# Optimization experiments

Hardware: AMD Instinct MI355X
Metric: run time of the kernel (lower is better)

Reference implementation:

```python
import jax, jax.numpy as jnp
import numpy as np

V, D, H, L, DF = 32000, 768, 12, 12, 3072
B, S, BS = 2, 1024, 16
MASK_ID = V - 1
HD = D // H
STD = 0.02


def setup_inputs() -> dict:
    key = jax.random.key(0)
    ks = jax.random.split(key, 12)
    ids = jax.random.randint(ks[0], (B, S), 0, V)
    m = jax.random.uniform(ks[1], (B, S)) < 0.15
    input_ids = jnp.where(m, MASK_ID, ids)
    target_ids = jax.random.randint(ks[2], (B, S), 0, V)
    noise_level = jax.random.uniform(ks[3], (B,), minval=0.1, maxval=1.0)
    emb = jax.random.normal(ks[4], (V, D)) * STD
    in_w = jax.random.normal(ks[5], (L, 3 * D, D)) * STD
    in_b = jnp.zeros((L, 3 * D))
    attn_out_w = jax.random.normal(ks[6], (L, D, D)) * STD
    attn_out_b = jnp.zeros((L, D))
    ln1_w = jnp.ones((L, D)); ln1_b = jnp.zeros((L, D))
    ln2_w = jnp.ones((L, D)); ln2_b = jnp.zeros((L, D))
    w1 = jax.random.normal(ks[7], (L, DF, D)) * STD; b1 = jnp.zeros((L, DF))
    w2 = jax.random.normal(ks[8], (L, D, DF)) * STD; b2 = jnp.zeros((L, D))
    proj_w = jax.random.normal(ks[9], (V, D)) * STD; proj_b = jnp.zeros((V,))
    return dict(input_ids=input_ids, target_ids=target_ids, noise_level=noise_level,
                emb=emb, in_w=in_w, in_b=in_b, attn_out_w=attn_out_w, attn_out_b=attn_out_b,
                ln1_w=ln1_w, ln1_b=ln1_b, ln2_w=ln2_w, ln2_b=ln2_b,
                w1=w1, b1=b1, w2=w2, b2=b2, proj_w=proj_w, proj_b=proj_b)


def _ln(x, w, b):
    m = x.mean(-1, keepdims=True)
    v = ((x - m) ** 2).mean(-1, keepdims=True)
    return (x - m) / jnp.sqrt(v + 1e-5) * w + b


def _rotary(x):
    # Vectorized equivalent of the per-scalar torch loop: rotates pairs
    # (0,1),(2,3),... within the first rotary_dim = D//2 channels only.
    rd = D // 2
    freqs = 1.0 / (10000.0 ** (jnp.arange(0, rd, 2, dtype=jnp.float32) / rd))  # [rd//2]
    ang = jnp.arange(S, dtype=jnp.float32)[:, None] * freqs[None, :]           # [S, rd//2]
    cos, sin = jnp.cos(ang), jnp.sin(ang)
    xr = x[..., :rd].reshape(B, S, rd // 2, 2)
    x0, x1 = xr[..., 0], xr[..., 1]
    r0 = x0 * cos - x1 * sin
    r1 = x0 * sin + x1 * cos
    rot = jnp.stack([r0, r1], axis=-1).reshape(B, S, rd)
    return jnp.concatenate([rot, x[..., rd:]], axis=-1)


def _block_causal_mask():
    nb = S // BS
    bm = jnp.tril(jnp.ones((nb, nb), dtype=jnp.float32))
    em = jnp.repeat(jnp.repeat(bm, BS, axis=0), BS, axis=1)  # [S, S]
    return (1.0 - em) * -1e9


def _model(input_ids, target_ids, noise_level, emb, in_w, in_b, attn_out_w, attn_out_b,
           ln1_w, ln1_b, ln2_w, ln2_b, w1, b1, w2, b2, proj_w, proj_b):
    x = emb[input_ids]                 # [B, S, D]
    x = _rotary(x)
    mask = _block_causal_mask()        # [S, S] additive
    scale = 1.0 / jnp.sqrt(jnp.float32(HD))
    for l in range(L):
        h = _ln(x, ln1_w[l], ln1_b[l])
        qkv = h @ in_w[l].T + in_b[l]
        q, k, v = jnp.split(qkv, 3, axis=-1)
        q = q.reshape(B, S, H, HD).transpose(0, 2, 1, 3)
        k = k.reshape(B, S, H, HD).transpose(0, 2, 1, 3)
        v = v.reshape(B, S, H, HD).transpose(0, 2, 1, 3)
        scores = jnp.einsum('bhqd,bhkd->bhqk', q, k) * scale + mask
        a = jax.nn.softmax(scores, axis=-1)
        o = jnp.einsum('bhqk,bhkd->bhqd', a, v).transpose(0, 2, 1, 3).reshape(B, S, D)
        x = x + (o @ attn_out_w[l].T + attn_out_b[l])
        h = _ln(x, ln2_w[l], ln2_b[l])
        x = x + (jax.nn.gelu(h @ w1[l].T + b1[l], approximate=False) @ w2[l].T + b2[l])
    logits = x @ proj_w.T + proj_b     # [B, S, V]
    logp = jax.nn.log_softmax(logits, axis=-1)
    ce = -jnp.take_along_axis(logp, target_ids[..., None], axis=-1)[..., 0]  # [B, S]
    is_masked = (input_ids == MASK_ID).astype(logits.dtype)
    weighted = ce * is_masked / noise_level[:, None]
    loss = weighted.sum() / (is_masked.sum() + 1e-8)
    return loss, logits


def reference(input_ids, target_ids, noise_level, emb, in_w, in_b, attn_out_w, attn_out_b,
              ln1_w, ln1_b, ln2_w, ln2_b, w1, b1, w2, b2, proj_w, proj_b):
    return _model(input_ids, target_ids, noise_level, emb, in_w, in_b, attn_out_w, attn_out_b,
                  ln1_w, ln1_b, ln2_w, ln2_b, w1, b1, w2, b2, proj_w, proj_b)
```

## Files before the change

### kernel.cpp

```cpp
#include <hip/hip_runtime.h>
#include <hip/hip_bf16.h>
#include <math.h>

#define V_SZ 32000
#define D_SZ 768
#define H_SZ 12
#define L_SZ 12
#define DF_SZ 3072
#define B_SZ 2
#define S_SZ 1024
#define BS_SZ 16
#define HD_SZ 64
#define MASK_ID 31999
#define NTOK (B_SZ * S_SZ)

typedef __attribute__((ext_vector_type(8))) short bf16x8;
typedef __attribute__((ext_vector_type(4))) short bf16x4;
typedef __attribute__((ext_vector_type(4))) float f32x4;

union B8 { bf16x8 v; __hip_bfloat162 h[4]; };
union B4 { bf16x4 v; __hip_bfloat162 h[2]; };
union U4 { ushort4 u; __hip_bfloat162 h[2]; };
union U4E { ushort4 u; unsigned short e[4]; };

__device__ inline unsigned short f2bf(float x) {
    __hip_bfloat16 b = __float2bfloat16(x);
    union { __hip_bfloat16 b; unsigned short u; } c; c.b = b;
    return c.u;
}

__global__ __launch_bounds__(256) void conv_fold_kernel(
    const float* __restrict__ Wsrc, const float* __restrict__ lnw,
    const float* __restrict__ lnb, const float* __restrict__ bsrc,
    unsigned short* __restrict__ Wdst, float* __restrict__ bdst,
    int rows_per_layer)
{
    const int gw = (blockIdx.x * 256 + threadIdx.x) >> 6;
    const int lane = threadIdx.x & 63;
    const int l = gw / rows_per_layer;
    const float* src = Wsrc + (size_t)gw * D_SZ;
    const float* wv = lnw + l * D_SZ;
    const float* bv = lnb + l * D_SZ;
    unsigned short* dst = Wdst + (size_t)gw * D_SZ;
    float acc = 0.f;
#pragma unroll
    for (int j = 0; j < 3; ++j) {
        int k = lane * 4 + j * 256;
        float4 s = *(const float4*)(src + k);
        float4 w = *(const float4*)(wv + k);
        float4 bb = *(const float4*)(bv + k);
        acc += bb.x * s.x + bb.y * s.y + bb.z * s.z + bb.w * s.w;
        U4 o;
        o.h[0] = __float22bfloat162_rn(float2{s.x * w.x, s.y * w.y});
        o.h[1] = __float22bfloat162_rn(float2{s.z * w.z, s.w * w.w});
        *(ushort4*)(dst + k) = o.u;
    }
#pragma unroll
    for (int off = 32; off; off >>= 1) acc += __shfl_xor(acc, off);
    if (lane == 0) bdst[gw] = bsrc[gw] + acc;
}

__global__ __launch_bounds__(256) void conv_cast_kernel(
    const float* __restrict__ src, unsigned short* __restrict__ dst, int n8)
{
    int i = blockIdx.x * 256 + threadIdx.x;
    if (i >= n8) return;
    const float* p = src + (size_t)i * 8;
    float4 v0 = *(const float4*)p;
    float4 v1 = *(const float4*)(p + 4);
    B8 r;
    r.h[0] = __float22bfloat162_rn(float2{v0.x, v0.y});
    r.h[1] = __float22bfloat162_rn(float2{v0.z, v0.w});
    r.h[2] = __float22bfloat162_rn(float2{v1.x, v1.y});
    r.h[3] = __float22bfloat162_rn(float2{v1.z, v1.w});
    *(bf16x8*)(dst + (size_t)i * 8) = r.v;
}

__global__ __launch_bounds__(256) void embed_rot_kernel(
    const int* __restrict__ ids, const float* __restrict__ emb,
    float* __restrict__ x)
{
    const int tok = blockIdx.x;
    const int s = tok & (S_SZ - 1);
    const int id = ids[tok];
    const float* e = emb + (size_t)id * D_SZ;
    float* xo = x + (size_t)tok * D_SZ;
    const int t = threadIdx.x;

    if (t < 192) {
        float x0 = e[2 * t], x1 = e[2 * t + 1];
        float freq = powf(10000.f, -((float)(2 * t)) / 384.f);
        float ang = (float)s * freq;
        float sn, cs;
        sincosf(ang, &sn, &cs);
        xo[2 * t]     = x0 * cs - x1 * sn;
        xo[2 * t + 1] = x0 * sn + x1 * cs;
    }
    for (int ch = 384 + t; ch < D_SZ; ch += 256) xo[ch] = e[ch];
}

template<int BM, int BN, int AM, int CM, bool WB16, bool XSWZ, bool CEP, int SPLITK>
__global__ __launch_bounds__(256) void mfma_gemm(
    const void* __restrict__ Av, const void* __restrict__ Wv,
    const float* __restrict__ bias, const float* __restrict__ Res,
    float* __restrict__ C,
    unsigned short* __restrict__ qp, unsigned short* __restrict__ kp,
    unsigned short* __restrict__ vp, float2* __restrict__ pm,
    int M, int N, int K)
{
    constexpr int MR = BM / 32;
    constexpr int NR = BN / 32;
    constexpr int ACH = BM * 4 / 256;
    constexpr int BCH = BN * 4 / 256;

    __shared__ __align__(16) unsigned short As[2][BM * 32];
    __shared__ __align__(16) unsigned short Bs[2][BN * 32];
    __shared__ float smean[AM == 1 ? BM : 1];
    __shared__ float srstd[AM == 1 ? BM : 1];

    const int tid = threadIdx.x;
    const int lane = tid & 63;
    const int wave = tid >> 6;
    const int wrow0 = (wave >> 1) * (BM / 2);
    const int wcol0 = (wave & 1) * (BN / 2);
    const int kgrp = lane >> 4;
    const int rc = lane & 15;
    const int dsw = ((kgrp - (rc >> 1)) & 3) * 8;

    int m0, n0;
    if constexpr (XSWZ) {
        int id = blockIdx.y * gridDim.x + blockIdx.x;
        int cpx = (gridDim.x * gridDim.y) >> 3;
        int swz = (id & 7) * cpx + (id >> 3);
        m0 = (swz % gridDim.x) * BM;
        n0 = (swz / gridDim.x) * BN;
    } else {
        m0 = blockIdx.x * BM;
        n0 = blockIdx.y * BN;
    }
    const int kdiv = K / SPLITK;
    const int kbase = (SPLITK > 1) ? blockIdx.z * kdiv : 0;

    if constexpr (AM == 1) {
        const float* A = (const float*)Av;
        const int row = tid >> 2, q = tid & 3;
        const float* xr = A + (size_t)(m0 + row) * K + q * (K >> 2);
        float sum = 0.f, ss = 0.f;
        for (int j = 0; j < (K >> 4); ++j) {
            float4 v = *(const float4*)(xr + j * 4);
            sum += v.x + v.y + v.z + v.w;
            ss += v.x * v.x + v.y * v.y + v.z * v.z + v.w * v.w;
        }
        sum += __shfl_xor(sum, 1); sum += __shfl_xor(sum, 2);
        ss  += __shfl_xor(ss, 1);  ss  += __shfl_xor(ss, 2);
        float mean = sum * (1.f / (float)K);
        float var = ss * (1.f / (float)K) - mean * mean;
        if (q == 0) { smean[row] = mean; srstd[row] = rsqrtf(var + 1e-5f); }
        __syncthreads();
    }

    f32x4 acc[MR][NR];
#pragma unroll
    for (int i = 0; i < MR; ++i)
#pragma unroll
        for (int j = 0; j < NR; ++j) acc[i][j] = (f32x4){0.f, 0.f, 0.f, 0.f};

    float areg[(AM != 2) ? ACH : 1][8];
    bf16x8 areg16[(AM == 2) ? ACH : 1];
    float bregf[WB16 ? 1 : BCH][8];
    bf16x8 breg16[WB16 ? BCH : 1];

    auto load_a = [&](int k0) {
#pragma unroll
        for (int i = 0; i < ACH; ++i) {
            int c = tid + i * 256;
            int row = c >> 2, ksg = ((c & 3) + (c >> 3)) & 3;
            if constexpr (AM == 2) {
                const unsigned short* A16 = (const unsigned short*)Av;
                areg16[i] = *(const bf16x8*)(A16 + (size_t)(m0 + row) * K + k0 + ksg * 8);
            } else {
                const float* p = (const float*)Av + (size_t)(m0 + row) * K + k0 + ksg * 8;
                float4 v0 = *(const float4*)p;
                float4 v1 = *(const float4*)(p + 4);
                areg[i][0] = v0.x; areg[i][1] = v0.y; areg[i][2] = v0.z; areg[i][3] = v0.w;
                areg[i][4] = v1.x; areg[i][5] = v1.y; areg[i][6] = v1.z; areg[i][7] = v1.w;
            }
        }
    };
    auto write_a = [&](int buf) {
#pragma unroll
        for (int i = 0; i < ACH; ++i) {
            int c = tid + i * 256;
            if constexpr (AM == 2) {
                *(bf16x8*)&As[buf][c * 8] = areg16[i];
            } else {
                int row = c >> 2;
                float sc = 1.f, sh = 0.f;
                if constexpr (AM == 1) { sc = srstd[row]; sh = -smean[row] * sc; }
                B8 r;
                r.h[0] = __float22bfloat162_rn(float2{fmaf(areg[i][0], sc, sh), fmaf(areg[i][1], sc, sh)});
                r.h[1] = __float22bfloat162_rn(float2{fmaf(areg[i][2], sc, sh), fmaf(areg[i][3], sc, sh)});
                r.h[2] = __float22bfloat162_rn(float2{fmaf(areg[i][4], sc, sh), fmaf(areg[i][5], sc, sh)});
                r.h[3] = __float22bfloat162_rn(float2{fmaf(areg[i][6], sc, sh), fmaf(areg[i][7], sc, sh)});
                *(bf16x8*)&As[buf][c * 8] = r.v;
            }
        }
    };

    auto load_b = [&](int k0) {
#pragma unroll
        for (int i = 0; i < BCH; ++i) {
            int c = tid + i * 256;
            int row = c >> 2, ksg = ((c & 3) + (c >> 3)) & 3;
            if constexpr (WB16) {
                const unsigned short* W16 = (const unsigned short*)Wv;
                breg16[i] = *(const bf16x8*)(W16 + (size_t)(n0 + row) * K + k0 + ksg * 8);
            } else {
                const float* p = (const float*)Wv + (size_t)(n0 + row) * K + k0 + ksg * 8;
                float4 v0 = *(const float4*)p;
                float4 v1 = *(const float4*)(p + 4);
                bregf[i][0] = v0.x; bregf[i][1] = v0.y; bregf[i][2] = v0.z; bregf[i][3] = v0.w;
                bregf[i][4] = v1.x; bregf[i][5] = v1.y; bregf[i][6] = v1.z; bregf[i][7] = v1.w;
            }
        }
    };
    auto write_b = [&](int buf) {
#pragma unroll
        for (int i = 0; i < BCH; ++i) {
            int c = tid + i * 256;
            if constexpr (WB16) {
                *(bf16x8*)&Bs[buf][c * 8] = breg16[i];
            } else {
                B8 r;
                r.h[0] = __float22bfloat162_rn(float2{bregf[i][0], bregf[i][1]});
                r.h[1] = __float22bfloat162_rn(float2{bregf[i][2], bregf[i][3]});
                r.h[2] = __float22bfloat162_rn(float2{bregf[i][4], bregf[i][5]});
                r.h[3] = __float22bfloat162_rn(float2{bregf[i][6], bregf[i][7]});
                *(bf16x8*)&Bs[buf][c * 8] = r.v;
            }
        }
    };

    auto compute = [&](int buf) {
        bf16x8 af[MR], bf[NR];
#pragma unroll
        for (int mi = 0; mi < MR; ++mi)
            af[mi] = *(const bf16x8*)&As[buf][(wrow0 + mi * 16 + rc) * 32 + dsw];
#pragma unroll
        for (int ni = 0; ni < NR; ++ni)
            bf[ni] = *(const bf16x8*)&Bs[buf][(wcol0 + ni * 16 + rc) * 32 + dsw];
#pragma unroll
        for (int mi = 0; mi < MR; ++mi)
#pragma unroll
            for (int ni = 0; ni < NR; ++ni)
                acc[mi][ni] = __builtin_amdgcn_mfma_f32_16x16x32_bf16(
                    af[mi], bf[ni], acc[mi][ni], 0, 0, 0);
    };

    load_a(kbase);
    load_b(kbase);
    write_a(0);
    write_b(0);
    __syncthreads();

    const int nk = kdiv >> 5;
    int cur = 0;
    for (int s = 0; s < nk; ++s) {
        const bool more = (s + 1 < nk);
        const int k1 = kbase + ((s + 1) << 5);
        if (more) { load_a(k1); load_b(k1); }
        compute(cur);
        if (more) { write_a(cur ^ 1); write_b(cur ^ 1); }
        __syncthreads();
        cur ^= 1;
    }

#pragma unroll
    for (int mi = 0; mi < MR; ++mi) {
#pragma unroll
        for (int ni = 0; ni < NR; ++ni) {
            const int col = n0 + wcol0 + ni * 16 + rc;
            const int rbase = m0 + wrow0 + mi * 16 + kgrp * 4;
            if constexpr (CM == 1) {
                float bv = bias[col];
                const int region = col / 768;
                const int c768 = col - region * 768;
                const int hh = c768 >> 6, d = c768 & 63;
                const int bb = rbase >> 10, s0 = rbase & 1023;
                const int bh = bb * H_SZ + hh;
                if (region == 0) {
#pragma unroll
                    for (int i = 0; i < 4; ++i)
                        qp[((size_t)(bh << 10) + s0 + i) * 64 + d]
                            = f2bf((acc[mi][ni][i] + bv) * 0.125f);
                } else if (region == 1) {
#pragma unroll
                    for (int i = 0; i < 4; ++i)
                        kp[((size_t)(bh << 10) + s0 + i) * 64 + d]
                            = f2bf(acc[mi][ni][i] + bv);
                } else {
                    U4E t4;
#pragma unroll
                    for (int i = 0; i < 4; ++i) t4.e[i] = f2bf(acc[mi][ni][i] + bv);
                    *(ushort4*)&vp[(((size_t)bh * 64 + d) << 10) + s0] = t4.u;
                }
            } else if constexpr (CM == 2) {
                float bv = bias[col];
                unsigned short* C16 = (unsigned short*)C;
#pragma unroll
                for (int i = 0; i < 4; ++i) {
                    float v = acc[mi][ni][i] + bv;
                    v = 0.5f * v * (1.f + erff(v * 0.70710678118654752f));
                    C16[(size_t)(rbase + i) * N + col] = f2bf(v);
                }
            } else if constexpr (CM == 3) {
                float* P = C + (size_t)blockIdx.z * ((size_t)M * N);
                size_t basei = (size_t)rbase * N + col;
#pragma unroll
                for (int i = 0; i < 4; ++i)
                    P[basei + (size_t)i * N] = acc[mi][ni][i];
            } else {
                float bv = bias ? bias[col] : 0.f;
                size_t basei = (size_t)rbase * N + col;
#pragma unroll
                for (int i = 0; i < 4; ++i) {
                    float v = acc[mi][ni][i] + bv;
                    size_t idx = basei + (size_t)i * N;
                    if (Res) v += Res[idx];
                    C[idx] = v;
                }
            }
        }
    }

    if constexpr (CEP) {
        float2 (*sce)[2] = (float2 (*)[2])As;
        float bvv[NR];
#pragma unroll
        for (int ni = 0; ni < NR; ++ni) bvv[ni] = bias[n0 + wcol0 + ni * 16 + rc];
#pragma unroll
        for (int mi = 0; mi < MR; ++mi) {
#pragma unroll
            for (int i = 0; i < 4; ++i) {
                float vmax = -1e30f;
#pragma unroll
                for (int ni = 0; ni < NR; ++ni)
                    vmax = fmaxf(vmax, acc[mi][ni][i] + bvv[ni]);
                vmax = fmaxf(vmax, __shfl_xor(vmax, 1));
                vmax = fmaxf(vmax, __shfl_xor(vmax, 2));
                vmax = fmaxf(vmax, __shfl_xor(vmax, 4));
                vmax = fmaxf(vmax, __shfl_xor(vmax, 8));
                float ssum = 0.f;
#pragma unroll
                for (int ni = 0; ni < NR; ++ni)
                    ssum += __expf(acc[mi][ni][i] + bvv[ni] - vmax);
                ssum += __shfl_xor(ssum, 1);
                ssum += __shfl_xor(ssum, 2);
                ssum += __shfl_xor(ssum, 4);
                ssum += __shfl_xor(ssum, 8);
                if (rc == 0)
                    sce[wrow0 + mi * 16 + kgrp * 4 + i][wave & 1] = float2{vmax, ssum};
            }
        }
        __syncthreads();
        if (tid < BM) {
            float2 a = sce[tid][0], b2 = sce[tid][1];
            float Mv = fmaxf(a.x, b2.x);
            float Sv = a.y * __expf(a.x - Mv) + b2.y * __expf(b2.x - Mv);
            pm[(size_t)(n0 >> 7) * NTOK + m0 + tid] = float2{Mv, Sv};
        }
    }
}

__global__ __launch_bounds__(256) void ffn2_reduce_kernel(
    const float* __restrict__ pp, const float* __restrict__ bias,
    float* __restrict__ x)
{
    const size_t i = (size_t)(blockIdx.x * 256 + threadIdx.x) * 8;
    const int col = (int)(i % 768);
    const size_t E = (size_t)NTOK * D_SZ;
    float4 s0 = *(const float4*)(x + i);
    float4 s1 = *(const float4*)(x + i + 4);
    float4 b0 = *(const float4*)(bias + col);
    float4 b1 = *(const float4*)(bias + col + 4);
    s0.x += b0.x; s0.y += b0.y; s0.z += b0.z; s0.w += b0.w;
    s1.x += b1.x; s1.y += b1.y; s1.z += b1.z; s1.w += b1.w;
#pragma unroll
    for (int z = 0; z < 2; ++z) {
        float4 p0 = *(const float4*)(pp + z * E + i);
        float4 p1 = *(const float4*)(pp + z * E + i + 4);
        s0.x += p0.x; s0.y += p0.y; s0.z += p0.z; s0.w += p0.w;
        s1.x += p1.x; s1.y += p1.y; s1.z += p1.z; s1.w += p1.w;
    }
    *(float4*)(x + i) = s0;
    *(float4*)(x + i + 4) = s1;
}

__global__ __launch_bounds__(256) void attn3_kernel(
    const unsigned short* __restrict__ Q16, const unsigned short* __restrict__ K16,
    const unsigned short* __restrict__ VT16, unsigned short* __restrict__ ao16)
{
    const int bid = blockIdx.x;
    const int qb = 63 - bid / 24;
    const int bh = bid % 24;
    const int b = bh / H_SZ, h = bh % H_SZ;
    const int tid = threadIdx.x;
    const int w = tid >> 6, lane = tid & 63;
    const int g = lane >> 4, r = lane & 15;

    constexpr int KS = 72;
    __shared__ __align__(16) unsigned short Pl[4][16 * KS];
    __shared__ float so[4][16][66];
    __shared__ float2 sml[4][16];

    const unsigned short* Qb = Q16 + ((size_t)bh << 10) * 64;
    const unsigned short* Kb = K16 + ((size_t)bh << 10) * 64;
    const unsigned short* Vb = VT16 + ((size_t)bh << 6) * 1024;

    bf16x8 qf[2];
    qf[0] = *(const bf16x8*)&Qb[(qb * 16 + r) * 64 + 8 * g];
    qf[1] = *(const bf16x8*)&Qb[(qb * 16 + r) * 64 + 32 + 8 * g];

    float m_r = -1e30f, l_r = 0.f;
    f32x4 o[4];
#pragma unroll
    for (int ni = 0; ni < 4; ++ni) o[ni] = (f32x4){0.f, 0.f, 0.f, 0.f};

    const int nch = (qb >> 2) + 1;
    const int qbm = qb & 3;

    for (int c = w; c < nch; c += 4) {
        const bool lastc = (c == nch - 1);
        const int mi_hi = lastc ? qbm : 3;

        f32x4 s[4];
#pragma unroll
        for (int mi = 0; mi < 4; ++mi) s[mi] = (f32x4){0.f, 0.f, 0.f, 0.f};
#pragma unroll
        for (int mi = 0; mi < 4; ++mi) {
            if (mi <= mi_hi) {
#pragma unroll
                for (int ks = 0; ks < 2; ++ks) {
                    bf16x8 af = *(const bf16x8*)&Kb[(c * 64 + 16 * mi + r) * 64 + 32 * ks + 8 * g];
                    s[mi] = __builtin_amdgcn_mfma_f32_16x16x32_bf16(af, qf[ks], s[mi], 0, 0, 0);
                }
            }
        }

        float mx = -1e30f;
#pragma unroll
        for (int mi = 0; mi < 4; ++mi) {
            if (mi <= mi_hi) {
#pragma unroll
                for (int i = 0; i < 4; ++i) mx = fmaxf(mx, s[mi][i]);
            }
        }
        mx = fmaxf(mx, __shfl_xor(mx, 16));
        mx = fmaxf(mx, __shfl_xor(mx, 32));
        float m_new = fmaxf(m_r, mx);
        float corr = __expf(m_r - m_new);

        float p[4][4];
        float psum = 0.f;
#pragma unroll
        for (int mi = 0; mi < 4; ++mi) {
#pragma unroll
            for (int i = 0; i < 4; ++i) {
                float pv = (mi <= mi_hi) ? __expf(s[mi][i] - m_new) : 0.f;
                p[mi][i] = pv;
                psum += pv;
            }
        }
        psum += __shfl_xor(psum, 16);
        psum += __shfl_xor(psum, 32);
        l_r = l_r * corr + psum;
        m_r = m_new;

#pragma unroll
        for (int mi = 0; mi < 4; ++mi) {
            B4 t;
            t.h[0] = __float22bfloat162_rn(float2{p[mi][0], p[mi][1]});
            t.h[1] = __float22bfloat162_rn(float2{p[mi][2], p[mi][3]});
            *(bf16x4*)&Pl[w][r * KS + 16 * mi + 4 * g] = t.v;
        }

        float co[4];
#pragma unroll
        for (int i = 0; i < 4; ++i) co[i] = __shfl(corr, 4 * g + i);
#pragma unroll
        for (int ni = 0; ni < 4; ++ni)
#pragma unroll
            for (int i = 0; i < 4; ++i) o[ni][i] *= co[i];

#pragma unroll
        for (int ks = 0; ks < 2; ++ks) {
            if (!lastc || 2 * ks <= qbm) {
                bf16x8 pf = *(const bf16x8*)&Pl[w][r * KS + 32 * ks + 8 * g];
#pragma unroll
                for (int ni = 0; ni < 4; ++ni) {
                    bf16x8 vf = *(const bf16x8*)&Vb[(size_t)(r + 16 * ni) * 1024 + c * 64 + 32 * ks + 8 * g];
                    o[ni] = __builtin_amdgcn_mfma_f32_16x16x32_bf16(pf, vf, o[ni], 0, 0, 0);
                }
            }
        }
    }

    if (g == 0) sml[w][r] = float2{m_r, l_r};
#pragma unroll
    for (int ni = 0; ni < 4; ++ni)
#pragma unroll
        for (int i = 0; i < 4; ++i)
            so[w][4 * g + i][r + 16 * ni] = o[ni][i];
    __syncthreads();

#pragma unroll
    for (int j = 0; j < 4; ++j) {
        int e = tid + j * 256;
        int row = e >> 6, col = e & 63;
        float2 p0 = sml[0][row], p1 = sml[1][row], p2 = sml[2][row], p3 = sml[3][row];
        float M = fmaxf(fmaxf(p0.x, p1.x), fmaxf(p2.x, p3.x));
        float w0 = __expf(p0.x - M), w1 = __expf(p1.x - M);
        float w2 = __expf(p2.x - M), w3 = __expf(p3.x - M);
        float L = p0.y * w0 + p1.y * w1 + p2.y * w2 + p3.y * w3;
        float ov = so[0][row][col] * w0 + so[1][row][col] * w1
                 + so[2][row][col] * w2 + so[3][row][col] * w3;
        ao16[(size_t)(b * S_SZ + qb * 16 + row) * D_SZ + h * HD_SZ + col]
            = f2bf(ov / L);
    }
}

__global__ __launch_bounds__(256) void ce2_kernel(
    const float* __restrict__ logits, const int* __restrict__ tgt,
    const int* __restrict__ inp, const float* __restrict__ noise,
    float* __restrict__ ce_row, float* __restrict__ msk_row)
{
    const int row = blockIdx.x;
    const int t = threadIdx.x;
    const float* lr = logits + (size_t)row * V_SZ;
    const float4* lr4 = (const float4*)lr;

    float m = -1e30f, s = 0.f;
    for (int i = t; i < V_SZ / 4; i += 256) {
        float4 v = lr4[i];
        float mx4 = fmaxf(fmaxf(v.x, v.y), fmaxf(v.z, v.w));
        if (mx4 > m) { s *= __expf(m - mx4); m = mx4; }
        s += __expf(v.x - m) + __expf(v.y - m) + __expf(v.z - m) + __expf(v.w - m);
    }

    __shared__ float sm[256], ss[256];
    sm[t] = m; ss[t] = s;
    __syncthreads();
    for (int off = 128; off; off >>= 1) {
        if (t < off) {
            float m2 = fmaxf(sm[t], sm[t + off]);
            ss[t] = ss[t] * __expf(sm[t] - m2) + ss[t + off] * __expf(sm[t + off] - m2);
            sm[t] = m2;
        }
        __syncthreads();
    }
    if (t == 0) {
        float M = sm[0], S = ss[0];
        int tg = tgt[row];
        float ce = -(lr[tg] - M - logf(S));
        int ism = (inp[row] == MASK_ID) ? 1 : 0;
        int b = row / S_SZ;
        ce_row[row] = ism ? (ce / noise[b]) : 0.f;
        msk_row[row] = ism ? 1.f : 0.f;
    }
}

__global__ __launch_bounds__(64) void ce3_kernel(
    const float2* __restrict__ pm, const float* __restrict__ logits,
    const int* __restrict__ tgt, const int* __restrict__ inp,
    const float* __restrict__ noise, float* __restrict__ ce_row,
    float* __restrict__ msk_row)
{
    const int row = blockIdx.x * 64 + threadIdx.x;
    float m = -1e30f, s = 0.f;
    for (int bb = 0; bb < V_SZ / 128; ++bb) {
        float2 p = pm[(size_t)bb * NTOK + row];
        float M2 = fmaxf(m, p.x);
        s = s * __expf(m - M2) + p.y * __expf(p.x - M2);
        m = M2;
    }
    int tg = tgt[row];
    float lv = logits[(size_t)row * V_SZ + tg];
    float ce = -(lv - m - logf(s));
    int ism = (inp[row] == MASK_ID) ? 1 : 0;
    int b = row / S_SZ;
    ce_row[row] = ism ? (ce / noise[b]) : 0.f;
    msk_row[row] = ism ? 1.f : 0.f;
}

__global__ __launch_bounds__(256) void loss_reduce_kernel(
    const float* __restrict__ ce_row, const float* __restrict__ msk_row,
    float* __restrict__ out0)
{
    const int t = threadIdx.x;
    __shared__ float r1[256], r2[256];
    float s = 0.f, c = 0.f;
    for (int i = t; i < NTOK; i += 256) { s += ce_row[i]; c += msk_row[i]; }
    r1[t] = s; r2[t] = c;
    __syncthreads();
    for (int off = 128; off; off >>= 1) {
        if (t < off) { r1[t] += r1[t + off]; r2[t] += r2[t + off]; }
        __syncthreads();
    }
    if (t == 0) out0[0] = r1[0] / (r2[0] + 1e-8f);
}

extern "C" void kernel_launch(void* const* d_in, const int* in_sizes, int n_in,
                              void* d_out, int out_size, void* d_ws, size_t ws_size,
                              hipStream_t stream)
{
    const int*   input_ids  = (const int*)d_in[0];
    const int*   target_ids = (const int*)d_in[1];
    const float* noise      = (const float*)d_in[2];
    const float* emb        = (const float*)d_in[3];
    const float* in_w       = (const float*)d_in[4];
    const float* in_b       = (const float*)d_in[5];
    const float* aow        = (const float*)d_in[6];
    const float* aob        = (const float*)d_in[7];
    const float* ln1w       = (const float*)d_in[8];
    const float* ln1b       = (const float*)d_in[9];
    const float* ln2w       = (const float*)d_in[10];
    const float* ln2b       = (const float*)d_in[11];
    const float* w1         = (const float*)d_in[12];
    const float* b1         = (const float*)d_in[13];
    const float* w2         = (const float*)d_in[14];
    const float* b2         = (const float*)d_in[15];
    const float* projw      = (const float*)d_in[16];
    const float* projb      = (const float*)d_in[17];

    float* out    = (float*)d_out;
    float* logits = out + 1;

    float* base = out + 4;
    unsigned short* wq16 = (unsigned short*)(base);
    unsigned short* wa16 = (unsigned short*)(base + 10616832);
    unsigned short* w116 = (unsigned short*)(base + 14155776);
    unsigned short* w216 = (unsigned short*)(base + 28311552);
    float* qkvb2 = base + 42467328;
    float* b1b2  = qkvb2 + 27648;
    unsigned short* Q16  = (unsigned short*)(base + 42531840);
    unsigned short* K16  = (unsigned short*)(base + 43318272);
    unsigned short* VT16 = (unsigned short*)(base + 44104704);
    unsigned short* ao16 = (unsigned short*)(base + 44891136);
    unsigned short* mid16= (unsigned short*)(base + 45677568);
    float* pp            = base + 48823296;

    float* x       = (float*)d_ws;
    float* ce_row  = x + (size_t)NTOK * D_SZ;
    float* msk_row = ce_row + NTOK;
    unsigned short* xb16 = (unsigned short*)(msk_row + NTOK);
    unsigned short* projw16 = xb16 + (size_t)NTOK * D_SZ;
    float2* pm = (float2*)d_ws;
    const bool fA = ws_size >= 9453568ull;
    const bool fB = ws_size >= 58605568ull;

    conv_fold_kernel<<<6912, 256, 0, stream>>>(in_w, ln1w, ln1b, in_b, wq16, qkvb2, 2304);
    conv_fold_kernel<<<9216, 256, 0, stream>>>(w1, ln2w, ln2b, b1, w116, b1b2, 3072);
    conv_cast_kernel<<<3456, 256, 0, stream>>>(aow, wa16, 884736);
    conv_cast_kernel<<<13824, 256, 0, stream>>>(w2, w216, 3538944);
    if (fB)
        conv_cast_kernel<<<12000, 256, 0, stream>>>(projw, projw16, 3072000);

    embed_rot_kernel<<<NTOK, 256, 0, stream>>>(input_ids, emb, x);

    for (int l = 0; l < L_SZ; ++l) {
        mfma_gemm<64, 128, 1, 1, true, false, false, 1><<<dim3(32, 18), 256, 0, stream>>>(
            x, wq16 + (size_t)l * 1769472, qkvb2 + l * 2304, nullptr, nullptr,
            Q16, K16, VT16, nullptr, NTOK, 2304, 768);
        attn3_kernel<<<1536, 256, 0, stream>>>(Q16, K16, VT16, ao16);
        mfma_gemm<64, 64, 2, 0, true, false, false, 1><<<dim3(32, 12), 256, 0, stream>>>(
            ao16, wa16 + (size_t)l * 589824, aob + l * D_SZ, x, x,
            nullptr, nullptr, nullptr, nullptr, NTOK, 768, 768);
        mfma_gemm<64, 128, 1, 2, true, false, false, 1><<<dim3(32, 24), 256, 0, stream>>>(
            x, w116 + (size_t)l * 2359296, b1b2 + l * 3072, nullptr, (float*)mid16,
            nullptr, nullptr, nullptr, nullptr, NTOK, 3072, 768);
        mfma_gemm<64, 64, 2, 3, true, false, false, 2><<<dim3(32, 12, 2), 256, 0, stream>>>(
            mid16, w216 + (size_t)l * 2359296, nullptr, nullptr, pp,
            nullptr, nullptr, nullptr, nullptr, NTOK, 768, 3072);
        ffn2_reduce_kernel<<<768, 256, 0, stream>>>(pp, b2 + l * D_SZ, x);
    }

    if (fA)
        conv_cast_kernel<<<768, 256, 0, stream>>>(x, xb16, 196608);

    if (fB) {
        mfma_gemm<128, 128, 2, 0, true, true, true, 1><<<dim3(16, 250), 256, 0, stream>>>(
            xb16, projw16, projb, nullptr, logits,
            nullptr, nullptr, nullptr, pm, NTOK, V_SZ, 768);
        ce3_kernel<<<32, 64, 0, stream>>>(pm, logits, target_ids, input_ids,
                                          noise, ce_row, msk_row);
    } else if (fA) {
        mfma_gemm<128, 128, 2, 0, false, true, true, 1><<<dim3(16, 250), 256, 0, stream>>>(
            xb16, projw, projb, nullptr, logits,
            nullptr, nullptr, nullptr, pm, NTOK, V_SZ, 768);
        ce3_kernel<<<32, 64, 0, stream>>>(pm, logits, target_ids, input_ids,
                                          noise, ce_row, msk_row);
    } else {
        mfma_gemm<128, 128, 0, 0, false, true, false, 1><<<dim3(16, 250), 256, 0, stream>>>(
            x, projw, projb, nullptr, logits,
            nullptr, nullptr, nullptr, nullptr, NTOK, V_SZ, 768);
        ce2_kernel<<<NTOK, 256, 0, stream>>>(logits, target_ids, input_ids, noise,
                                             ce_row, msk_row);
    }

    loss_reduce_kernel<<<1, 256, 0, stream>>>(ce_row, msk_row, out);
}
```

Before: 2.535 ms.

## Precompute LayerNorm row stats in residual-reduce kernels; split-K attention out-proj

The embedding kernel and a new per-row reduce kernel now compute each row's LayerNorm mean and rstd once and write them to a small stats buffer. The LN-folded GEMMs read these stats instead of recomputing them, which previously had every N-tile block rescan the full fp32 rows. The attention output projection now runs split-K=2 into partial buffers, followed by a reduce kernel that adds residual and bias and computes stats. This adds one launch per layer and more partial-buffer traffic, and the new reduce kernel uses one block per row with scalar loads.

New measurement: 2.199 ms. 13.2% less time.

```diff
diff --git a/kernel.cpp b/kernel.cpp
--- a/kernel.cpp
+++ b/kernel.cpp
@@ -78,7 +78,7 @@
 
 __global__ __launch_bounds__(256) void embed_rot_kernel(
     const int* __restrict__ ids, const float* __restrict__ emb,
-    float* __restrict__ x)
+    float* __restrict__ x, float2* __restrict__ stats)
 {
     const int tok = blockIdx.x;
     const int s = tok & (S_SZ - 1);
@@ -87,16 +87,73 @@
     float* xo = x + (size_t)tok * D_SZ;
     const int t = threadIdx.x;
 
+    float sum = 0.f, ssum = 0.f;
     if (t < 192) {
         float x0 = e[2 * t], x1 = e[2 * t + 1];
         float freq = powf(10000.f, -((float)(2 * t)) / 384.f);
         float ang = (float)s * freq;
         float sn, cs;
         sincosf(ang, &sn, &cs);
-        xo[2 * t]     = x0 * cs - x1 * sn;
-        xo[2 * t + 1] = x0 * sn + x1 * cs;
-    }
-    for (int ch = 384 + t; ch < D_SZ; ch += 256) xo[ch] = e[ch];
+        float r0 = x0 * cs - x1 * sn;
+        float r1 = x0 * sn + x1 * cs;
+        xo[2 * t]     = r0;
+        xo[2 * t + 1] = r1;
+        sum += r0 + r1; ssum += r0 * r0 + r1 * r1;
+    }
+    {
+        float e1 = e[384 + t];
+        xo[384 + t] = e1;
+        sum += e1; ssum += e1 * e1;
+    }
+    if (t < 128) {
+        float e2 = e[640 + t];
+        xo[640 + t] = e2;
+        sum += e2; ssum += e2 * e2;
+    }
+
+    __shared__ float r1s[256], r2s[256];
+    r1s[t] = sum; r2s[t] = ssum;
+    __syncthreads();
+    for (int off = 128; off; off >>= 1) {
+        if (t < off) { r1s[t] += r1s[t + off]; r2s[t] += r2s[t + off]; }
+        __syncthreads();
+    }
+    if (t == 0) {
+        float mean = r1s[0] * (1.f / 768.f);
+        float var = r2s[0] * (1.f / 768.f) - mean * mean;
+        stats[tok] = float2{mean, rsqrtf(var + 1e-5f)};
+    }
+}
+
+__global__ __launch_bounds__(256) void reduce_ln_kernel(
+    const float* __restrict__ pp, const float* __restrict__ bias,
+    float* __restrict__ x, float2* __restrict__ stats)
+{
+    const int row = blockIdx.x;
+    const int t = threadIdx.x;
+    const size_t base = (size_t)row * D_SZ;
+    const size_t E = (size_t)NTOK * D_SZ;
+
+    float sum = 0.f, ssum = 0.f;
+#pragma unroll
+    for (int j = 0; j < 3; ++j) {
+        int c = t + 256 * j;
+        float v = x[base + c] + bias[c] + pp[base + c] + pp[E + base + c];
+        x[base + c] = v;
+        sum += v; ssum += v * v;
+    }
+    __shared__ float r1s[256], r2s[256];
+    r1s[t] = sum; r2s[t] = ssum;
+    __syncthreads();
+    for (int off = 128; off; off >>= 1) {
+        if (t < off) { r1s[t] += r1s[t + off]; r2s[t] += r2s[t + off]; }
+        __syncthreads();
+    }
+    if (t == 0) {
+        float mean = r1s[0] * (1.f / 768.f);
+        float var = r2s[0] * (1.f / 768.f) - mean * mean;
+        stats[row] = float2{mean, rsqrtf(var + 1e-5f)};
+    }
 }
 
 template<int BM, int BN, int AM, int CM, bool WB16, bool XSWZ, bool CEP, int SPLITK>
@@ -106,6 +163,7 @@
     float* __restrict__ C,
     unsigned short* __restrict__ qp, unsigned short* __restrict__ kp,
     unsigned short* __restrict__ vp, float2* __restrict__ pm,
+    const float2* __restrict__ stats,
     int M, int N, int K)
 {
     constexpr int MR = BM / 32;
@@ -142,20 +200,10 @@
     const int kbase = (SPLITK > 1) ? blockIdx.z * kdiv : 0;
 
     if constexpr (AM == 1) {
-        const float* A = (const float*)Av;
-        const int row = tid >> 2, q = tid & 3;
-        const float* xr = A + (size_t)(m0 + row) * K + q * (K >> 2);
-        float sum = 0.f, ss = 0.f;
-        for (int j = 0; j < (K >> 4); ++j) {
-            float4 v = *(const float4*)(xr + j * 4);
-            sum += v.x + v.y + v.z + v.w;
-            ss += v.x * v.x + v.y * v.y + v.z * v.z + v.w * v.w;
-        }
-        sum += __shfl_xor(sum, 1); sum += __shfl_xor(sum, 2);
-        ss  += __shfl_xor(ss, 1);  ss  += __shfl_xor(ss, 2);
-        float mean = sum * (1.f / (float)K);
-        float var = ss * (1.f / (float)K) - mean * mean;
-        if (q == 0) { smean[row] = mean; srstd[row] = rsqrtf(var + 1e-5f); }
+        if (tid < BM) {
+            float2 st = stats[m0 + tid];
+            smean[tid] = st.x; srstd[tid] = st.y;
+        }
         __syncthreads();
     }
 
@@ -370,30 +418,6 @@
             pm[(size_t)(n0 >> 7) * NTOK + m0 + tid] = float2{Mv, Sv};
         }
     }
-}
-
-__global__ __launch_bounds__(256) void ffn2_reduce_kernel(
-    const float* __restrict__ pp, const float* __restrict__ bias,
-    float* __restrict__ x)
-{
-    const size_t i = (size_t)(blockIdx.x * 256 + threadIdx.x) * 8;
-    const int col = (int)(i % 768);
-    const size_t E = (size_t)NTOK * D_SZ;
-    float4 s0 = *(const float4*)(x + i);
-    float4 s1 = *(const float4*)(x + i + 4);
-    float4 b0 = *(const float4*)(bias + col);
-    float4 b1 = *(const float4*)(bias + col + 4);
-    s0.x += b0.x; s0.y += b0.y; s0.z += b0.z; s0.w += b0.w;
-    s1.x += b1.x; s1.y += b1.y; s1.z += b1.z; s1.w += b1.w;
-#pragma unroll
-    for (int z = 0; z < 2; ++z) {
-        float4 p0 = *(const float4*)(pp + z * E + i);
-        float4 p1 = *(const float4*)(pp + z * E + i + 4);
-        s0.x += p0.x; s0.y += p0.y; s0.z += p0.z; s0.w += p0.w;
-        s1.x += p1.x; s1.y += p1.y; s1.z += p1.z; s1.w += p1.w;
-    }
-    *(float4*)(x + i) = s0;
-    *(float4*)(x + i + 4) = s1;
 }
 
 __global__ __launch_bounds__(256) void attn3_kernel(
@@ -652,11 +676,12 @@
     float* x       = (float*)d_ws;
     float* ce_row  = x + (size_t)NTOK * D_SZ;
     float* msk_row = ce_row + NTOK;
-    unsigned short* xb16 = (unsigned short*)(msk_row + NTOK);
+    float2* stats  = (float2*)(msk_row + NTOK);
+    unsigned short* xb16 = (unsigned short*)(msk_row + NTOK + 2 * NTOK);
     unsigned short* projw16 = xb16 + (size_t)NTOK * D_SZ;
     float2* pm = (float2*)d_ws;
-    const bool fA = ws_size >= 9453568ull;
-    const bool fB = ws_size >= 58605568ull;
+    const bool fA = ws_size >= 9469952ull;
+    const bool fB = ws_size >= 58621952ull;
 
     conv_fold_kernel<<<6912, 256, 0, stream>>>(in_w, ln1w, ln1b, in_b, wq16, qkvb2, 2304);
     conv_fold_kernel<<<9216, 256, 0, stream>>>(w1, ln2w, ln2b, b1, w116, b1b2, 3072);
@@ -665,23 +690,24 @@
     if (fB)
         conv_cast_kernel<<<12000, 256, 0, stream>>>(projw, projw16, 3072000);
 
-    embed_rot_kernel<<<NTOK, 256, 0, stream>>>(input_ids, emb, x);
+    embed_rot_kernel<<<NTOK, 256, 0, stream>>>(input_ids, emb, x, stats);
 
     for (int l = 0; l < L_SZ; ++l) {
         mfma_gemm<64, 128, 1, 1, true, false, false, 1><<<dim3(32, 18), 256, 0, stream>>>(
             x, wq16 + (size_t)l * 1769472, qkvb2 + l * 2304, nullptr, nullptr,
-            Q16, K16, VT16, nullptr, NTOK, 2304, 768);
+            Q16, K16, VT16, nullptr, stats, NTOK, 2304, 768);
         attn3_kernel<<<1536, 256, 0, stream>>>(Q16, K16, VT16, ao16);
-        mfma_gemm<64, 64, 2, 0, true, false, false, 1><<<dim3(32, 12), 256, 0, stream>>>(
-            ao16, wa16 + (size_t)l * 589824, aob + l * D_SZ, x, x,
-            nullptr, nullptr, nullptr, nullptr, NTOK, 768, 768);
+        mfma_gemm<64, 64, 2, 3, true, false, false, 2><<<dim3(32, 12, 2), 256, 0, stream>>>(
+            ao16, wa16 + (size_t)l * 589824, nullptr, nullptr, pp,
+            nullptr, nullptr, nullptr, nullptr, nullptr, NTOK, 768, 768);
+        reduce_ln_kernel<<<NTOK, 256, 0, stream>>>(pp, aob + l * D_SZ, x, stats);
         mfma_gemm<64, 128, 1, 2, true, false, false, 1><<<dim3(32, 24), 256, 0, stream>>>(
             x, w116 + (size_t)l * 2359296, b1b2 + l * 3072, nullptr, (float*)mid16,
-            nullptr, nullptr, nullptr, nullptr, NTOK, 3072, 768);
+            nullptr, nullptr, nullptr, nullptr, stats, NTOK, 3072, 768);
         mfma_gemm<64, 64, 2, 3, true, false, false, 2><<<dim3(32, 12, 2), 256, 0, stream>>>(
             mid16, w216 + (size_t)l * 2359296, nullptr, nullptr, pp,
-            nullptr, nullptr, nullptr, nullptr, NTOK, 768, 3072);
-        ffn2_reduce_kernel<<<768, 256, 0, stream>>>(pp, b2 + l * D_SZ, x);
+            nullptr, nullptr, nullptr, nullptr, nullptr, NTOK, 768, 3072);
+        reduce_ln_kernel<<<NTOK, 256, 0, stream>>>(pp, b2 + l * D_SZ, x, stats);
     }
 
     if (fA)
@@ -690,19 +716,19 @@
     if (fB) {
         mfma_gemm<128, 128, 2, 0, true, true, true, 1><<<dim3(16, 250), 256, 0, stream>>>(
             xb16, projw16, projb, nullptr, logits,
-            nullptr, nullptr, nullptr, pm, NTOK, V_SZ, 768);
+            nullptr, nullptr, nullptr, pm, nullptr, NTOK, V_SZ, 768);
         ce3_kernel<<<32, 64, 0, stream>>>(pm, logits, target_ids, input_ids,
                                           noise, ce_row, msk_row);
     } else if (fA) {
         mfma_gemm<128, 128, 2, 0, false, true, true, 1><<<dim3(16, 250), 256, 0, stream>>>(
             xb16, projw, projb, nullptr, logits,
-            nullptr, nullptr, nullptr, pm, NTOK, V_SZ, 768);
+            nullptr, nullptr, nullptr, pm, nullptr, NTOK, V_SZ, 768);
         ce3_kernel<<<32, 64, 0, stream>>>(pm, logits, target_ids, input_ids,
                                           noise, ce_row, msk_row);
     } else {
         mfma_gemm<128, 128, 0, 0, false, true, false, 1><<<dim3(16, 250), 256, 0, stream>>>(
             x, projw, projb, nullptr, logits,
-            nullptr, nullptr, nullptr, nullptr, NTOK, V_SZ, 768);
+            nullptr, nullptr, nullptr, nullptr, nullptr, NTOK, V_SZ, 768);
         ce2_kernel<<<NTOK, 256, 0, stream>>>(logits, target_ids, input_ids, noise,
                                              ce_row, msk_row);
     }
```
